# Optimization experiments

Hardware: AMD Instinct MI355X
Metric: run time of the kernel (lower is better)

Reference implementation:

```python
import math
import jax, jax.numpy as jnp
import numpy as np
from jax import lax

TAU = 1.0
LAMBDA_COUNT = 1.0
ALPHA = 0.85
GAMMA = 1.0
NUM_ITER = 40


def _minpool(x, wh, ww):
    # equals -max_pool2d(-x) in torch (padding acts as +inf for min)
    return lax.reduce_window(x, jnp.inf, lax.min, (1, 1, wh, ww), (1, 1, 1, 1),
                             [(0, 0), (0, 0), (wh // 2, wh // 2), (ww // 2, ww // 2)])


def _maxpool(x, wh, ww):
    return lax.reduce_window(x, -jnp.inf, lax.max, (1, 1, wh, ww), (1, 1, 1, 1),
                             [(0, 0), (0, 0), (wh // 2, wh // 2), (ww // 2, ww // 2)])


def soft_erode(img):
    return jnp.minimum(_minpool(img, 3, 1), _minpool(img, 1, 3))


def soft_dilate(img):
    return _maxpool(img, 3, 3)


def soft_open(img):
    return soft_dilate(soft_erode(img))


def soft_skel(img):
    skel = jax.nn.relu(img - soft_open(img))

    def step(carry, _):
        img, skel = carry
        img = soft_erode(img)
        delta = jax.nn.relu(img - soft_open(img))
        skel = skel + jax.nn.relu(delta - skel * delta)
        return (img, skel), None

    (_, skel), _ = lax.scan(step, (img, skel), None, length=NUM_ITER)
    return skel


def soft_endpoints(skel):
    kernel = jnp.ones((3, 3), dtype=skel.dtype).at[1, 1].set(10.0)[None, None]  # OIHW
    neighbor_sum = lax.conv_general_dilated(skel, kernel, (1, 1), [(1, 1), (1, 1)],
                                            dimension_numbers=('NCHW', 'OIHW', 'NCHW'))
    return jnp.exp(-GAMMA * (neighbor_sum - 11.0) ** 2) * skel


def weighted_coordinates(ep):
    # ep: [B,1,H,W] -> [B,2] (y,x) weighted mean coordinates
    B, _, H, W = ep.shape
    ys = jnp.arange(H, dtype=ep.dtype)
    xs = jnp.arange(W, dtype=ep.dtype)
    total = jnp.sum(ep, axis=(1, 2, 3)) + 1e-8  # [B]
    w = ep[:, 0] / total[:, None, None]  # [B,H,W]
    yc = jnp.sum(w * ys[:, None], axis=(1, 2))
    xc = jnp.sum(w * xs[None, :], axis=(1, 2))
    return jnp.stack([yc, xc], axis=1)


def soft_dice(y_true, y_pred):
    smooth = 1.0
    inter = jnp.sum(y_true * y_pred)
    coeff = (2.0 * inter + smooth) / (jnp.sum(y_true) + jnp.sum(y_pred) + smooth)
    return 1.0 - coeff


def setup_inputs() -> dict:
    key = jax.random.key(0)
    k1, k2 = jax.random.split(key)
    network_output = jax.random.normal(k1, (8, 2, 512, 512), dtype=jnp.float32)
    y_true = jax.random.randint(k2, (8, 1, 512, 512), 0, 2).astype(jnp.int32)
    return {"network_output": network_output, "y_true": y_true}


def reference(network_output, y_true):
    B, _, H, W = network_output.shape
    pred_prob_fg = jax.nn.softmax(network_output, axis=1)[:, 1:2]  # [B,1,H,W]
    y_true_f = y_true.astype(pred_prob_fg.dtype)

    skel_pred = soft_skel(pred_prob_fg)
    skel_true = soft_skel(y_true_f)

    ep_pred = soft_endpoints(skel_pred)
    ep_true = soft_endpoints(skel_true)

    # mismatch (distance) term
    pred_coords = weighted_coordinates(ep_pred)  # [B,2]
    true_coords = weighted_coordinates(ep_true)
    dist = jnp.sqrt(jnp.sum((pred_coords - true_coords) ** 2, axis=1))
    unnormalized_distance_loss = jnp.mean(dist)

    image_diagonal = math.sqrt(H ** 2 + W ** 2)
    distance_loss = unnormalized_distance_loss / (image_diagonal * TAU + 1e-8)

    n_pred = jnp.sum(ep_pred, axis=(1, 2, 3))
    n_true = jnp.sum(ep_true, axis=(1, 2, 3))
    count_penalty = jnp.mean(jnp.abs(n_pred - n_true) / (n_pred + n_true + 1e-8))

    final_endpoint_loss = distance_loss + LAMBDA_COUNT * count_penalty
    dice = soft_dice(y_true_f, pred_prob_fg)
    return ALPHA * dice + (1.0 - ALPHA) * final_endpoint_loss
```

## Files before the change

### kernel.cpp

```cpp
#include <hip/hip_runtime.h>
#include <math.h>

#define W 512
#define H 512
#define S (W * H)
#define B 8
#define NIMG 16
#define CORE_Y 128
#define CORE_X 64
#define HALO 12
#define LDT 88
#define TROWS 154
#define NQ 22
#define FINF __builtin_huge_valf()

__device__ __forceinline__ float4 ld4s(const float* p) { return *(const float4*)p; }
__device__ __forceinline__ void st4s(float* p, float4 v) { *(float4*)p = v; }

__device__ __forceinline__ float blockReduce(float v, float* sw) {
    #pragma unroll
    for (int o = 32; o; o >>= 1) v += __shfl_down(v, o, 64);
    int lane = threadIdx.x & 63, wid = threadIdx.x >> 6;
    if (lane == 0) sw[wid] = v;
    __syncthreads();
    float r = (threadIdx.x < 4) ? sw[threadIdx.x] : 0.f;
    if (wid == 0) { r += __shfl_down(r, 2, 64); r += __shfl_down(r, 1, 64); }
    __syncthreads();
    return r;
}

__global__ __launch_bounds__(256) void phase1_kernel(
        const float* __restrict__ net, const int* __restrict__ yt,
        float* __restrict__ J0, double* __restrict__ pb,
        double* __restrict__ acc) {
    __shared__ float sw[4];
    const int tid = threadIdx.x;
    if (blockIdx.x == 0 && tid < 48) acc[tid] = 0.0;
    float inter = 0.f, sp = 0.f, sy = 0.f;
    for (int i = blockIdx.x * 256 + tid; i < B * S / 4; i += 1024 * 256) {
        int b = i >> 16;
        int s = (i & 65535) << 2;
        const float* nb = net + (size_t)b * 2 * S;
        float4 x0 = ld4s(nb + s);
        float4 x1 = ld4s(nb + S + s);
        int4 yv = *(const int4*)(yt + (size_t)b * S + s);
        float4 p, yf;
        p.x = 1.f / (1.f + expf(x0.x - x1.x));
        p.y = 1.f / (1.f + expf(x0.y - x1.y));
        p.z = 1.f / (1.f + expf(x0.z - x1.z));
        p.w = 1.f / (1.f + expf(x0.w - x1.w));
        yf.x = (float)yv.x; yf.y = (float)yv.y; yf.z = (float)yv.z; yf.w = (float)yv.w;
        st4s(J0 + (size_t)b * S + s, p);
        st4s(J0 + (size_t)(B + b) * S + s, yf);
        inter += p.x * yf.x + p.y * yf.y + p.z * yf.z + p.w * yf.w;
        sp += p.x + p.y + p.z + p.w;
        sy += yf.x + yf.y + yf.z + yf.w;
    }
    float v;
    v = blockReduce(inter, sw); if (tid == 0) pb[blockIdx.x * 3 + 0] = (double)v;
    v = blockReduce(sp, sw);    if (tid == 0) pb[blockIdx.x * 3 + 1] = (double)v;
    v = blockReduce(sy, sw);    if (tid == 0) pb[blockIdx.x * 3 + 2] = (double)v;
}

template <bool INIT>
__global__ __launch_bounds__(512, 4) void skel_fused_kernel(
        const float* __restrict__ Jin, float* __restrict__ Jout,
        float* __restrict__ skel, int r0) {
    __shared__ float Jl[TROWS * LDT];
    const int tid = threadIdx.x;
    const int lane = tid & 63;
    const int img = blockIdx.x >> 5;
    const int t32 = blockIdx.x & 31;
    const int ty = t32 >> 3, tx = t32 & 7;
    const int y0 = ty * CORE_Y - HALO, x0 = tx * CORE_X - HALO;
    const float* Ji = Jin + (size_t)img * S;
    float* Jo = Jout + (size_t)img * S;
    float* Sk = skel + (size_t)img * S;
    const bool interior = (ty > 0) & (ty < 3) & (tx > 0) & (tx < 7);

    if (interior) {
        for (int i = tid; i < TROWS * NQ; i += 512) {
            int r = i / NQ, q = i - (i / NQ) * NQ;
            st4s(&Jl[r * LDT + (q << 2)],
                 ld4s(Ji + (y0 + r) * W + x0 + (q << 2)));
        }
    } else {
        for (int i = tid; i < TROWS * NQ; i += 512) {
            int r = i / NQ, q = i - (i / NQ) * NQ;
            int gy = y0 + r, gx = x0 + (q << 2);
            float4 v;
            if ((unsigned)gy < H && (unsigned)gx < W) v = ld4s(Ji + gy * W + gx);
            else v = make_float4(FINF, FINF, FINF, FINF);
            st4s(&Jl[r * LDT + (q << 2)], v);
        }
    }

    const int sq = tid & 15, ss = tid >> 4;
    const int tcol = HALO + (sq << 2);
    const int gxc = tx * CORE_X + (sq << 2);
    const int trow = HALO + (ss << 2);
    const int grow = ty * CORE_Y + (ss << 2);
    float4 sk4[4];
    #pragma unroll
    for (int j = 0; j < 4; ++j) {
        if (INIT) sk4[j] = make_float4(0.f, 0.f, 0.f, 0.f);
        else      sk4[j] = ld4s(Sk + (grow + j) * W + gxc);
    }
    __syncthreads();

    float4 Jc[4];
    #pragma unroll
    for (int j = 0; j < 4; ++j) Jc[j] = ld4s(Jl + (trow + j) * LDT + tcol);

    for (int rr = r0; rr < 6; ++rr) {
        const int rlo = 1 + 2 * rr;
        const int clo = 1 + 2 * rr, chi = 86 - 2 * rr;
        const int qlo = clo >> 2, qhi = chi >> 2;
        const int nq = qhi - qlo + 1;
        const int nslab = (152 - 4 * rr) >> 2;
        const int nit = nslab * nq;

        float4 Er[2][4];
        int rb_[2], cc_[2];
        bool act_[2];
        #pragma unroll
        for (int s2 = 0; s2 < 2; ++s2) {
            int it = tid + (s2 << 9);
            const bool act = (it < nit);
            act_[s2] = act;
            if (act) {
                int sb = it / nq;
                int qq = qlo + (it - sb * nq);
                int rb = rlo + (sb << 2);
                int cc = qq << 2;
                rb_[s2] = rb; cc_[s2] = cc;
                const float* bp = Jl + (rb - 1) * LDT + cc;
                float4 wA = ld4s(bp);
                float4 wB = ld4s(bp + LDT);
                const bool cOOB = (!interior) && ((unsigned)(x0 + cc) >= W);
                #pragma unroll
                for (int j = 0; j < 4; ++j) {
                    float4 wC = ld4s(bp + (j + 2) * LDT);
                    float lw = __shfl_up(wB.w, 1, 64);
                    float rx = __shfl_down(wB.x, 1, 64);
                    if (lane == 0 && qq != qlo)  lw = Jl[(rb + j) * LDT + cc - 1];
                    if (lane == 63 && qq != qhi) rx = Jl[(rb + j) * LDT + cc + 4];
                    if (qq == qlo) lw = FINF;
                    if (qq == qhi) rx = FINF;
                    float4 e;
                    e.x = fminf(fminf(fminf(wA.x, wC.x), fminf(lw, wB.y)), wB.x);
                    e.y = fminf(fminf(fminf(wA.y, wC.y), fminf(wB.x, wB.z)), wB.y);
                    e.z = fminf(fminf(fminf(wA.z, wC.z), fminf(wB.y, wB.w)), wB.z);
                    e.w = fminf(fminf(fminf(wA.w, wC.w), fminf(wB.z, rx)), wB.w);
                    if (!interior) {
                        int gy = y0 + rb + j;
                        if (((unsigned)gy >= H) | cOOB)
                            e = make_float4(FINF, FINF, FINF, FINF);
                    }
                    Er[s2][j] = e;
                    wA = wB; wB = wC;
                }
            }
        }
        __syncthreads();

        #pragma unroll
        for (int s2 = 0; s2 < 2; ++s2) {
            if (act_[s2]) {
                #pragma unroll
                for (int j = 0; j < 4; ++j)
                    st4s(&Jl[(rb_[s2] + j) * LDT + cc_[s2]], Er[s2][j]);
            }
        }
        __syncthreads();

        const bool last = (rr == 5);
        {
            const float* ebase = Jl + (trow - 1) * LDT + tcol;
            float4 E[6];
            #pragma unroll
            for (int j = 0; j < 6; ++j) E[j] = ld4s(ebase + j * LDT);
            float lwv[6], rxv[6];
            #pragma unroll
            for (int j = 0; j < 6; ++j) {
                lwv[j] = __shfl_up(E[j].w, 1, 64);
                rxv[j] = __shfl_down(E[j].x, 1, 64);
                if (sq == 0)  lwv[j] = (tx == 0) ? -FINF : Jl[(trow - 1 + j) * LDT + 11];
                if (sq == 15) rxv[j] = (tx == 7) ? -FINF : Jl[(trow - 1 + j) * LDT + 76];
            }
            float4 hx[6];
            #pragma unroll
            for (int j = 0; j < 6; ++j) {
                hx[j].x = fmaxf(fmaxf(lwv[j], E[j].x), E[j].y);
                hx[j].y = fmaxf(fmaxf(E[j].x, E[j].y), E[j].z);
                hx[j].z = fmaxf(fmaxf(E[j].y, E[j].z), E[j].w);
                hx[j].w = fmaxf(fmaxf(E[j].z, E[j].w), rxv[j]);
            }
            #pragma unroll
            for (int j = 0; j < 4; ++j) {
                int gy = grow + j;
                float4 hm = hx[j], hp = hx[j + 2];
                if (!interior) {
                    if (gy == 0)     hm = make_float4(-FINF, -FINF, -FINF, -FINF);
                    if (gy == H - 1) hp = make_float4(-FINF, -FINF, -FINF, -FINF);
                }
                float4 dm;
                dm.x = fmaxf(fmaxf(hm.x, hx[j + 1].x), hp.x);
                dm.y = fmaxf(fmaxf(hm.y, hx[j + 1].y), hp.y);
                dm.z = fmaxf(fmaxf(hm.z, hx[j + 1].z), hp.z);
                dm.w = fmaxf(fmaxf(hm.w, hx[j + 1].w), hp.w);
                float4 Jv = Jc[j];
                float d0 = fmaxf(Jv.x - dm.x, 0.f);
                float d1 = fmaxf(Jv.y - dm.y, 0.f);
                float d2 = fmaxf(Jv.z - dm.z, 0.f);
                float d3 = fmaxf(Jv.w - dm.w, 0.f);
                sk4[j].x += fmaxf(d0 - sk4[j].x * d0, 0.f);
                sk4[j].y += fmaxf(d1 - sk4[j].y * d1, 0.f);
                sk4[j].z += fmaxf(d2 - sk4[j].z * d2, 0.f);
                sk4[j].w += fmaxf(d3 - sk4[j].w * d3, 0.f);
                Jc[j] = E[j + 1];
                if (last) {
                    st4s(Jo + gy * W + gxc, E[j + 1]);
                    st4s(Sk + gy * W + gxc, sk4[j]);
                }
            }
        }
        if (!last) __syncthreads();
    }
}

__global__ __launch_bounds__(256) void endpoint_kernel(
        const float* __restrict__ skel, double* __restrict__ acc) {
    __shared__ float sR[10][520];
    __shared__ float sw[4];
    const int tid = threadIdx.x;
    const int img = blockIdx.x >> 6;
    const int rb = blockIdx.x & 63;
    const int yB = rb << 3;
    const float* Sk = skel + (size_t)img * S;
    for (int i = tid; i < 1280; i += 256) {
        int r = i >> 7, c4 = i & 127;
        int gy = yB - 1 + r;
        float4 v = make_float4(0.f, 0.f, 0.f, 0.f);
        if ((unsigned)gy < H) v = ld4s(Sk + gy * W + (c4 << 2));
        st4s(&sR[r][4 + (c4 << 2)], v);
    }
    if (tid < 10) { sR[tid][3] = 0.f; sR[tid][516] = 0.f; }
    __syncthreads();
    float t = 0.f, syA = 0.f, sxA = 0.f;
    #pragma unroll
    for (int k = 0; k < 4; ++k) {
        int qidx = k * 256 + tid;
        int rrow = qidx >> 7;
        int x = (qidx & 127) << 2;
        int r = 1 + rrow;
        float gy = (float)(yB + rrow);
        const float* Rm = &sR[r - 1][4 + x];
        const float* Rc = &sR[r][4 + x];
        const float* Rp = &sR[r + 1][4 + x];
        float4 bm = ld4s(Rm); float lm = ld4s(Rm - 4).w, rm = ld4s(Rm + 4).x;
        float4 bc = ld4s(Rc); float lc = ld4s(Rc - 4).w, rc = ld4s(Rc + 4).x;
        float4 bp = ld4s(Rp); float lp = ld4s(Rp - 4).w, rp = ld4s(Rp + 4).x;
        float hm0 = lm + bm.x + bm.y, hm1 = bm.x + bm.y + bm.z;
        float hm2 = bm.y + bm.z + bm.w, hm3 = bm.z + bm.w + rm;
        float hc0 = lc + bc.x + bc.y, hc1 = bc.x + bc.y + bc.z;
        float hc2 = bc.y + bc.z + bc.w, hc3 = bc.z + bc.w + rc;
        float hp0 = lp + bp.x + bp.y, hp1 = bp.x + bp.y + bp.z;
        float hp2 = bp.y + bp.z + bp.w, hp3 = bp.z + bp.w + rp;
        float ns0 = hm0 + hc0 + hp0 + 9.f * bc.x;
        float ns1 = hm1 + hc1 + hp1 + 9.f * bc.y;
        float ns2 = hm2 + hc2 + hp2 + 9.f * bc.z;
        float ns3 = hm3 + hc3 + hp3 + 9.f * bc.w;
        float e0 = ns0 - 11.f, e1 = ns1 - 11.f, e2 = ns2 - 11.f, e3 = ns3 - 11.f;
        float ep0 = expf(-e0 * e0) * bc.x;
        float ep1 = expf(-e1 * e1) * bc.y;
        float ep2 = expf(-e2 * e2) * bc.z;
        float ep3 = expf(-e3 * e3) * bc.w;
        float es = ep0 + ep1 + ep2 + ep3;
        t += es;
        syA += gy * es;
        sxA += ep0 * (float)(x + 0) + ep1 * (float)(x + 1)
             + ep2 * (float)(x + 2) + ep3 * (float)(x + 3);
    }
    float v;
    v = blockReduce(t, sw);   if (tid == 0) atomicAdd(&acc[img * 3 + 0], (double)v);
    v = blockReduce(syA, sw); if (tid == 0) atomicAdd(&acc[img * 3 + 1], (double)v);
    v = blockReduce(sxA, sw); if (tid == 0) atomicAdd(&acc[img * 3 + 2], (double)v);
}

__global__ __launch_bounds__(256) void final_kernel(
        const double* __restrict__ acc, const double* __restrict__ pb,
        float* __restrict__ out) {
    const int tid = threadIdx.x;
    double si = 0.0, sp = 0.0, sy = 0.0;
    for (int i = tid; i < 1024; i += 256) {
        si += pb[i * 3 + 0]; sp += pb[i * 3 + 1]; sy += pb[i * 3 + 2];
    }
    #pragma unroll
    for (int o = 32; o; o >>= 1) {
        si += __shfl_down(si, o, 64);
        sp += __shfl_down(sp, o, 64);
        sy += __shfl_down(sy, o, 64);
    }
    __shared__ double dsw[3][4];
    int lane = tid & 63, wid = tid >> 6;
    if (lane == 0) { dsw[0][wid] = si; dsw[1][wid] = sp; dsw[2][wid] = sy; }
    __syncthreads();
    if (tid == 0) {
        double inter = dsw[0][0] + dsw[0][1] + dsw[0][2] + dsw[0][3];
        double sump  = dsw[1][0] + dsw[1][1] + dsw[1][2] + dsw[1][3];
        double sumy  = dsw[2][0] + dsw[2][1] + dsw[2][2] + dsw[2][3];
        double dsum = 0.0, csum = 0.0;
        for (int b = 0; b < B; ++b) {
            double tp = acc[b * 3 + 0], typ = acc[b * 3 + 1], txp = acc[b * 3 + 2];
            double tt = acc[(B + b) * 3 + 0], tyt = acc[(B + b) * 3 + 1], txt = acc[(B + b) * 3 + 2];
            double ycp = typ / (tp + 1e-8), xcp = txp / (tp + 1e-8);
            double yct = tyt / (tt + 1e-8), xct = txt / (tt + 1e-8);
            double dy = ycp - yct, dx = xcp - xct;
            dsum += sqrt(dy * dy + dx * dx);
            csum += fabs(tp - tt) / (tp + tt + 1e-8);
        }
        double diag = sqrt((double)(H * H + W * W));
        double distance_loss = (dsum / B) / (diag + 1e-8);
        double count_penalty = csum / B;
        double dice = 1.0 - (2.0 * inter + 1.0) / (sumy + sump + 1.0);
        out[0] = (float)(0.85 * dice + 0.15 * (distance_loss + count_penalty));
    }
}

extern "C" void kernel_launch(void* const* d_in, const int* in_sizes, int n_in,
                              void* d_out, int out_size, void* d_ws, size_t ws_size,
                              hipStream_t stream) {
    const float* net = (const float*)d_in[0];
    const int*   yt  = (const int*)d_in[1];
    float* out = (float*)d_out;

    float* J0   = (float*)d_ws;
    float* J1   = J0 + (size_t)NIMG * S;
    float* skel = J1 + (size_t)NIMG * S;
    double* acc = (double*)(skel + (size_t)NIMG * S);
    double* pb  = acc + 48;

    phase1_kernel<<<1024, 256, 0, stream>>>(net, yt, J0, pb, acc);

    skel_fused_kernel<true><<<NIMG * 32, 512, 0, stream>>>(J0, J1, skel, 0);
    float* a = J1; float* b = J0;
    for (int p = 1; p < 7; ++p) {
        int r0 = (p == 6) ? 1 : 0;
        skel_fused_kernel<false><<<NIMG * 32, 512, 0, stream>>>(a, b, skel, r0);
        float* tmp = a; a = b; b = tmp;
    }

    endpoint_kernel<<<NIMG * 64, 256, 0, stream>>>(skel, acc);
    final_kernel<<<1, 256, 0, stream>>>(acc, pb, out);
}
```

Measured before the change: 347.5 us.

## Use 64x64 tiles with fixed-size redundant halo erosion instead of shrinking regions

The skeleton kernel now uses 64x64 core tiles with 256 threads and twice as many blocks. It erodes the whole 90-row local tile every round instead of shrinking the computed region per round, which makes the index math uniform. Final J and skeleton stores move out of the loop to a single epilogue. The goal is more blocks and occupancy with cheaper indexing and fewer per-round branches. The cost is more redundant halo work per output pixel, since the halo is now a larger share of each tile.

```diff
diff --git a/kernel.cpp b/kernel.cpp
--- a/kernel.cpp
+++ b/kernel.cpp
@@ -6,11 +6,9 @@
 #define S (W * H)
 #define B 8
 #define NIMG 16
-#define CORE_Y 128
-#define CORE_X 64
-#define HALO 12
+#define CORE 64
 #define LDT 88
-#define TROWS 154
+#define LROWS 90
 #define NQ 22
 #define FINF __builtin_huge_valf()
 
@@ -63,31 +61,32 @@
 }
 
 template <bool INIT>
-__global__ __launch_bounds__(512, 4) void skel_fused_kernel(
+__global__ __launch_bounds__(256, 4) void skel_fused_kernel(
         const float* __restrict__ Jin, float* __restrict__ Jout,
-        float* __restrict__ skel, int r0) {
-    __shared__ float Jl[TROWS * LDT];
+        float* __restrict__ skel, int NR) {
+    __shared__ float Jl[LROWS * LDT];
     const int tid = threadIdx.x;
     const int lane = tid & 63;
-    const int img = blockIdx.x >> 5;
-    const int t32 = blockIdx.x & 31;
-    const int ty = t32 >> 3, tx = t32 & 7;
-    const int y0 = ty * CORE_Y - HALO, x0 = tx * CORE_X - HALO;
+    const int img = blockIdx.x >> 6;
+    const int t64 = blockIdx.x & 63;
+    const int ty = t64 >> 3, tx = t64 & 7;
+    const int yb = ty * CORE - 13;
+    const int x0 = tx * CORE - 12;
     const float* Ji = Jin + (size_t)img * S;
     float* Jo = Jout + (size_t)img * S;
     float* Sk = skel + (size_t)img * S;
-    const bool interior = (ty > 0) & (ty < 3) & (tx > 0) & (tx < 7);
+    const bool interior = (ty > 0) & (ty < 7) & (tx > 0) & (tx < 7);
 
     if (interior) {
-        for (int i = tid; i < TROWS * NQ; i += 512) {
+        for (int i = tid; i < LROWS * NQ; i += 256) {
             int r = i / NQ, q = i - (i / NQ) * NQ;
             st4s(&Jl[r * LDT + (q << 2)],
-                 ld4s(Ji + (y0 + r) * W + x0 + (q << 2)));
+                 ld4s(Ji + (yb + r) * W + x0 + (q << 2)));
         }
     } else {
-        for (int i = tid; i < TROWS * NQ; i += 512) {
+        for (int i = tid; i < LROWS * NQ; i += 256) {
             int r = i / NQ, q = i - (i / NQ) * NQ;
-            int gy = y0 + r, gx = x0 + (q << 2);
+            int gy = yb + r, gx = x0 + (q << 2);
             float4 v;
             if ((unsigned)gy < H && (unsigned)gx < W) v = ld4s(Ji + gy * W + gx);
             else v = make_float4(FINF, FINF, FINF, FINF);
@@ -96,10 +95,10 @@
     }
 
     const int sq = tid & 15, ss = tid >> 4;
-    const int tcol = HALO + (sq << 2);
-    const int gxc = tx * CORE_X + (sq << 2);
-    const int trow = HALO + (ss << 2);
-    const int grow = ty * CORE_Y + (ss << 2);
+    const int tcol = 12 + (sq << 2);
+    const int gxc = tx * CORE + (sq << 2);
+    const int trow = 13 + (ss << 2);
+    const int grow = ty * CORE + (ss << 2);
     float4 sk4[4];
     #pragma unroll
     for (int j = 0; j < 4; ++j) {
@@ -112,69 +111,59 @@
     #pragma unroll
     for (int j = 0; j < 4; ++j) Jc[j] = ld4s(Jl + (trow + j) * LDT + tcol);
 
-    for (int rr = r0; rr < 6; ++rr) {
-        const int rlo = 1 + 2 * rr;
-        const int clo = 1 + 2 * rr, chi = 86 - 2 * rr;
-        const int qlo = clo >> 2, qhi = chi >> 2;
-        const int nq = qhi - qlo + 1;
-        const int nslab = (152 - 4 * rr) >> 2;
-        const int nit = nslab * nq;
-
+    for (int rr = 0; rr < NR; ++rr) {
         float4 Er[2][4];
-        int rb_[2], cc_[2];
-        bool act_[2];
+        int rb2[2], cc2[2];
+        bool act2[2];
         #pragma unroll
         for (int s2 = 0; s2 < 2; ++s2) {
-            int it = tid + (s2 << 9);
-            const bool act = (it < nit);
-            act_[s2] = act;
-            if (act) {
-                int sb = it / nq;
-                int qq = qlo + (it - sb * nq);
-                int rb = rlo + (sb << 2);
-                int cc = qq << 2;
-                rb_[s2] = rb; cc_[s2] = cc;
-                const float* bp = Jl + (rb - 1) * LDT + cc;
-                float4 wA = ld4s(bp);
-                float4 wB = ld4s(bp + LDT);
-                const bool cOOB = (!interior) && ((unsigned)(x0 + cc) >= W);
-                #pragma unroll
-                for (int j = 0; j < 4; ++j) {
-                    float4 wC = ld4s(bp + (j + 2) * LDT);
-                    float lw = __shfl_up(wB.w, 1, 64);
-                    float rx = __shfl_down(wB.x, 1, 64);
-                    if (lane == 0 && qq != qlo)  lw = Jl[(rb + j) * LDT + cc - 1];
-                    if (lane == 63 && qq != qhi) rx = Jl[(rb + j) * LDT + cc + 4];
-                    if (qq == qlo) lw = FINF;
-                    if (qq == qhi) rx = FINF;
-                    float4 e;
-                    e.x = fminf(fminf(fminf(wA.x, wC.x), fminf(lw, wB.y)), wB.x);
-                    e.y = fminf(fminf(fminf(wA.y, wC.y), fminf(wB.x, wB.z)), wB.y);
-                    e.z = fminf(fminf(fminf(wA.z, wC.z), fminf(wB.y, wB.w)), wB.z);
-                    e.w = fminf(fminf(fminf(wA.w, wC.w), fminf(wB.z, rx)), wB.w);
-                    if (!interior) {
-                        int gy = y0 + rb + j;
-                        if (((unsigned)gy >= H) | cOOB)
-                            e = make_float4(FINF, FINF, FINF, FINF);
-                    }
-                    Er[s2][j] = e;
-                    wA = wB; wB = wC;
+            const int uraw = tid + (s2 << 8);
+            act2[s2] = (uraw < 484);
+            const int u = (uraw < 484) ? uraw : 483;
+            const int ei = u / 22;
+            const int eq = u - ei * 22;
+            const int rb = 1 + (ei << 2);
+            const int cc = eq << 2;
+            rb2[s2] = rb; cc2[s2] = cc;
+            const float* bp = Jl + (rb - 1) * LDT + cc;
+            float4 wA = ld4s(bp);
+            float4 wB = ld4s(bp + LDT);
+            const bool cOOB = (!interior) && ((unsigned)(x0 + cc) >= W);
+            #pragma unroll
+            for (int j = 0; j < 4; ++j) {
+                float4 wC = ld4s(bp + (j + 2) * LDT);
+                float lw = __shfl_up(wB.w, 1, 64);
+                float rx = __shfl_down(wB.x, 1, 64);
+                if (lane == 0 && eq > 0)   lw = Jl[(rb + j) * LDT + cc - 1];
+                if (lane == 63 && eq < 21) rx = Jl[(rb + j) * LDT + cc + 4];
+                if (eq == 0)  lw = FINF;
+                if (eq == 21) rx = FINF;
+                float4 e;
+                e.x = fminf(fminf(fminf(wA.x, wC.x), fminf(lw,   wB.y)), wB.x);
+                e.y = fminf(fminf(fminf(wA.y, wC.y), fminf(wB.x, wB.z)), wB.y);
+                e.z = fminf(fminf(fminf(wA.z, wC.z), fminf(wB.y, wB.w)), wB.z);
+                e.w = fminf(fminf(fminf(wA.w, wC.w), fminf(wB.z, rx  )), wB.w);
+                if (!interior) {
+                    int gy = yb + rb + j;
+                    if (((unsigned)gy >= H) | cOOB)
+                        e = make_float4(FINF, FINF, FINF, FINF);
                 }
+                Er[s2][j] = e;
+                wA = wB; wB = wC;
             }
         }
         __syncthreads();
 
         #pragma unroll
         for (int s2 = 0; s2 < 2; ++s2) {
-            if (act_[s2]) {
+            if (act2[s2]) {
                 #pragma unroll
                 for (int j = 0; j < 4; ++j)
-                    st4s(&Jl[(rb_[s2] + j) * LDT + cc_[s2]], Er[s2][j]);
+                    st4s(&Jl[(rb2[s2] + j) * LDT + cc2[s2]], Er[s2][j]);
             }
         }
         __syncthreads();
 
-        const bool last = (rr == 5);
         {
             const float* ebase = Jl + (trow - 1) * LDT + tcol;
             float4 E[6];
@@ -219,13 +208,15 @@
                 sk4[j].z += fmaxf(d2 - sk4[j].z * d2, 0.f);
                 sk4[j].w += fmaxf(d3 - sk4[j].w * d3, 0.f);
                 Jc[j] = E[j + 1];
-                if (last) {
-                    st4s(Jo + gy * W + gxc, E[j + 1]);
-                    st4s(Sk + gy * W + gxc, sk4[j]);
-                }
-            }
-        }
-        if (!last) __syncthreads();
+            }
+        }
+    }
+
+    #pragma unroll
+    for (int j = 0; j < 4; ++j) {
+        int gy = grow + j;
+        st4s(Jo + gy * W + gxc, Jc[j]);
+        st4s(Sk + gy * W + gxc, sk4[j]);
     }
 }
 
@@ -343,11 +334,11 @@
 
     phase1_kernel<<<1024, 256, 0, stream>>>(net, yt, J0, pb, acc);
 
-    skel_fused_kernel<true><<<NIMG * 32, 512, 0, stream>>>(J0, J1, skel, 0);
+    skel_fused_kernel<true><<<NIMG * 64, 256, 0, stream>>>(J0, J1, skel, 6);
     float* a = J1; float* b = J0;
     for (int p = 1; p < 7; ++p) {
-        int r0 = (p == 6) ? 1 : 0;
-        skel_fused_kernel<false><<<NIMG * 32, 512, 0, stream>>>(a, b, skel, r0);
+        int nr = (p == 6) ? 5 : 6;
+        skel_fused_kernel<false><<<NIMG * 64, 256, 0, stream>>>(a, b, skel, nr);
         float* tmp = a; a = b; b = tmp;
     }
 
```

New measurement: 338.3 us. -2.7%, faster.
